# Optimization experiments

Hardware: AMD Instinct MI355X
Metric: run time of the kernel (lower is better)

Reference implementation:

```python
import jax, jax.numpy as jnp
import numpy as np

N, E, G = 100000, 3_200_000, 128   # nodes, edges, graphs in batch
IN, H, C = 16, 64, 4               # in_dim, hidden, num_classes


def setup_inputs() -> dict:
    key = jax.random.key(0)
    ks = jax.random.split(key, 6)
    x = jax.random.normal(ks[0], (N, IN), dtype=jnp.float32)
    edge_index = jax.random.randint(ks[1], (2, E), 0, N, dtype=jnp.int64)
    batch = jnp.sort(jax.random.randint(ks[2], (N,), 0, G, dtype=jnp.int64))
    glorot = lambda k, shp, fan: jax.random.normal(k, shp, jnp.float32) / np.sqrt(fan).astype(np.float32)
    return dict(
        x=x, edge_index=edge_index, batch=batch,
        W1=glorot(ks[3], (IN, H), IN), b1=jnp.zeros((H,), jnp.float32),
        W2=glorot(ks[4], (H, H), H), b2=jnp.zeros((H,), jnp.float32),
        Wl=glorot(ks[5], (H, C), H), bl=jnp.zeros((C,), jnp.float32),
    )


def gcn_conv(x, src, dst, W, b, n):
    """PyG GCNConv: h = D^{-1/2} (A+I) D^{-1/2} (x W) + b, edges incl. self-loops."""
    h = x @ W  # [n, out]
    deg = jax.ops.segment_sum(jnp.ones(src.shape[0], x.dtype), dst, num_segments=n)
    dinv = jnp.where(deg > 0, jax.lax.rsqrt(deg), 0.0)
    norm = dinv[src] * dinv[dst]                       # [E+n]
    out = jax.ops.segment_sum(h[src] * norm[:, None], dst, num_segments=n)
    return out + b


def reference(x, edge_index, batch, W1, b1, W2, b2, Wl, bl):
    n = x.shape[0]
    loops = jnp.arange(n, dtype=edge_index.dtype)      # self-loops (gcn_norm)
    src = jnp.concatenate([edge_index[0], loops])
    dst = jnp.concatenate([edge_index[1], loops])
    h = jax.nn.relu(gcn_conv(x, src, dst, W1, b1, n))
    h = jax.nn.relu(gcn_conv(h, src, dst, W2, b2, n))
    g = jax.ops.segment_sum(h, batch, num_segments=G)  # global_add_pool -> [G, H]
    return g @ Wl + bl                                  # [G, C]
```

## Files before the change

### kernel.cpp

```cpp
#include <hip/hip_runtime.h>
#include <hip/hip_bf16.h>

#define NN 100000
#define EE 3200000
#define GG 128
#define IN_DIM 16
#define HDIM 64
#define CDIM 4

#define RN 256
#define NB ((NN + RN - 1) / RN)
#define CH 8192

typedef unsigned short u16;
typedef unsigned int u32;
typedef __attribute__((ext_vector_type(8))) short bf16x8;
typedef __attribute__((ext_vector_type(4))) float f32x4;

__device__ __forceinline__ float bf_lo(u32 w) { return __uint_as_float(w << 16); }
__device__ __forceinline__ float bf_hi(u32 w) { return __uint_as_float(w & 0xFFFF0000u); }
__device__ __forceinline__ u16 f2bf(float f) {
    u32 x = __float_as_uint(f);
    return (u16)((x + 0x7FFFu + ((x >> 16) & 1u)) >> 16);
}
__device__ __forceinline__ float rdlane(float v, int lane) {
    return __int_as_float(__builtin_amdgcn_readlane(__float_as_int(v), lane));
}


__global__ __launch_bounds__(512) void bhist_k(const int* __restrict__ dst,
                                               int* __restrict__ bcnt) {
    __shared__ int hist[NB];
    int t = threadIdx.x;
    long e0 = (long)blockIdx.x * CH;
    int cnt = (int)min((long)CH, (long)EE - e0);
    for (int i = t; i < NB; i += 512) hist[i] = 0;
    __syncthreads();
    for (int i = t; i < cnt; i += 512) atomicAdd(&hist[dst[e0 + i] >> 8], 1);
    __syncthreads();
    for (int i = t; i < NB; i += 512) {
        int v = hist[i];
        if (v > 0) atomicAdd(&bcnt[i], v);
    }
}

__global__ void bucketscan_k(const int* __restrict__ bcnt, int* __restrict__ bucketBase,
                             int* __restrict__ gcursor) {
    __shared__ int s[512];
    int t = threadIdx.x;
    int c = (t < NB) ? bcnt[t] : 0;
    s[t] = c;
    __syncthreads();
    for (int off = 1; off < 512; off <<= 1) {
        int v = (t >= off) ? s[t - off] : 0;
        __syncthreads();
        s[t] += v;
        __syncthreads();
    }
    if (t < NB) {
        int base = s[t] - c;
        bucketBase[t] = base;
        gcursor[t] = base;
    }
    if (t == 0) bucketBase[NB] = EE;
}


__global__ __launch_bounds__(512) void partition_k(const int* __restrict__ src,
                                                   const int* __restrict__ dst,
                                                   int* __restrict__ gcursor,
                                                   u32* __restrict__ pairs) {
    __shared__ int hist[NB];
    __shared__ int lbase[NB];
    __shared__ int gbase[NB];
    __shared__ int scanbuf[512];
    __shared__ u32 stag[CH];
    __shared__ u16 stagb[CH];
    int t = threadIdx.x;
    long e0 = (long)blockIdx.x * CH;
    int cnt = (int)min((long)CH, (long)EE - e0);

    for (int i = t; i < NB; i += 512) hist[i] = 0;
    __syncthreads();

    int myb[16], myloc[16];
    u32 myp[16];
#pragma unroll
    for (int r = 0; r < 16; ++r) {
        int i = t + (r << 9);
        if (i < cnt) {
            int s = src[e0 + i], d = dst[e0 + i];
            int b = d >> 8;
            myb[r] = b;
            myp[r] = ((u32)s << 8) | (u32)(d & 255);
            myloc[r] = atomicAdd(&hist[b], 1);
        } else {
            myb[r] = -1;
            myloc[r] = 0;
            myp[r] = 0;
        }
    }
    __syncthreads();

    scanbuf[t] = (t < NB) ? hist[t] : 0;
    __syncthreads();
    for (int off = 1; off < 512; off <<= 1) {
        int v = (t >= off) ? scanbuf[t - off] : 0;
        __syncthreads();
        scanbuf[t] += v;
        __syncthreads();
    }
    if (t < NB) {
        lbase[t] = scanbuf[t] - hist[t];
        gbase[t] = (hist[t] > 0) ? atomicAdd(&gcursor[t], hist[t]) : 0;
    }
    __syncthreads();

#pragma unroll
    for (int r = 0; r < 16; ++r) {
        if (myb[r] >= 0) {
            int pos = lbase[myb[r]] + myloc[r];
            stag[pos] = myp[r];
            stagb[pos] = (u16)myb[r];
        }
    }
    __syncthreads();

    for (int i = t; i < cnt; i += 512) {
        int b = stagb[i];
        pairs[gbase[b] + (i - lbase[b])] = stag[i];
    }
}


__global__ __launch_bounds__(512) void csrfill_k(const int* __restrict__ bucketBase,
                                                 const u32* __restrict__ pairs,
                                                 int* __restrict__ rowptr,
                                                 float* __restrict__ dinv,
                                                 int* __restrict__ srcS) {
    __shared__ int sb[256];
    __shared__ int sdeg[256];
    __shared__ int lcur[256];
    int b = blockIdx.x, t = threadIdx.x;
    int n0 = b << 8;
    int gb = bucketBase[b];
    int gend = bucketBase[b + 1];

    if (t < 256) sb[t] = 0;
    __syncthreads();

    for (int idx = gb + t; idx < gend; idx += 512) atomicAdd(&sb[pairs[idx] & 255u], 1);
    __syncthreads();

    int d = (t < 256) ? sb[t] : 0;
    if (t < 256) {
        sdeg[t] = d;
        int n = n0 + t;
        if (n < NN) dinv[n] = rsqrtf((float)(d + 1));
    }
    __syncthreads();
    for (int off = 1; off < 256; off <<= 1) {
        int v = 0;
        if (t < 256 && t >= off) v = sb[t - off];
        __syncthreads();
        if (t < 256) sb[t] += v;
        __syncthreads();
    }
    if (t < 256) {
        int excl = sb[t] - sdeg[t];
        int n = n0 + t;
        if (n < NN) rowptr[n] = gb + excl;
        lcur[t] = excl;
    }
    if (b == 0 && t == 0) rowptr[NN] = EE;
    __syncthreads();

    for (int idx = gb + t; idx < gend; idx += 512) {
        u32 p = pairs[idx];
        int dl = (int)(p & 255u);
        int slot = atomicAdd(&lcur[dl], 1);
        srcS[gb + slot] = (int)(p >> 8);
    }
}


__global__ void xs_k(const float* __restrict__ x, const float* __restrict__ dinv,
                     u16* __restrict__ xs) {
    int i = blockIdx.x * 256 + threadIdx.x;
    if (i >= NN * 4) return;
    int n = i >> 2;
    float dn = dinv[n];
    float4 v = ((const float4*)x)[i];
    u32 p0 = (u32)f2bf(v.x * dn) | ((u32)f2bf(v.y * dn) << 16);
    u32 p1 = (u32)f2bf(v.z * dn) | ((u32)f2bf(v.w * dn) << 16);
    uint2 pk; pk.x = p0; pk.y = p1;
    ((uint2*)xs)[i] = pk;
}

#define ACCUM8(acc, v)                       \
    {                                        \
        acc[0] += bf_lo(v.x);                \
        acc[1] += bf_hi(v.x);                \
        acc[2] += bf_lo(v.y);                \
        acc[3] += bf_hi(v.y);                \
        acc[4] += bf_lo(v.z);                \
        acc[5] += bf_hi(v.z);                \
        acc[6] += bf_lo(v.w);                \
        acc[7] += bf_hi(v.w);                \
    }

#define FOLD3(res, acc, mA, mB, mC)                                   \
    {                                                                 \
        float tj[4], uj[2];                                           \
        _Pragma("unroll")                                             \
        for (int j = 0; j < 4; j++) {                                 \
            float lo = acc[j], hi = acc[j + 4];                       \
            float snd = (lane & mA) ? lo : hi;                        \
            float rcv = __shfl_xor(snd, mA);                          \
            tj[j] = (lane & mA) ? hi + rcv : lo + rcv;                \
        }                                                             \
        _Pragma("unroll")                                             \
        for (int j = 0; j < 2; j++) {                                 \
            float lo = tj[j], hi = tj[j + 2];                         \
            float snd = (lane & mB) ? lo : hi;                        \
            float rcv = __shfl_xor(snd, mB);                          \
            uj[j] = (lane & mB) ? hi + rcv : lo + rcv;                \
        }                                                             \
        {                                                             \
            float lo = uj[0], hi = uj[1];                             \
            float snd = (lane & mC) ? lo : hi;                        \
            float rcv = __shfl_xor(snd, mC);                          \
            res = (lane & mC) ? hi + rcv : lo + rcv;                  \
        }                                                             \
    }


__global__ __launch_bounds__(256) void aggx_k(const u16* __restrict__ xs,
                                              const int* __restrict__ rowptr,
                                              const int* __restrict__ srcS,
                                              const float* __restrict__ dinv,
                                              const float* __restrict__ b1,
                                              const float* __restrict__ W1,
                                              u16* __restrict__ h1d) {
    int t = threadIdx.x;
    int lane = t & 63, w = t >> 6;
    int c = lane & 1, r = lane >> 1;
    int n0 = blockIdx.x * 8 + w * 2;
    int n1 = n0 + 1;

    float w1c[16];
#pragma unroll
    for (int k = 0; k < 16; k++) w1c[k] = W1[k * HDIM + lane];
    float b1l = b1[lane];

    int beg0 = rowptr[n0], end0 = rowptr[n0 + 1], end1 = rowptr[n0 + 2];
    int beg1 = end0;
    float dn0 = dinv[n0], dn1 = dinv[n1];

    float acc0[8] = {0, 0, 0, 0, 0, 0, 0, 0};
    float acc1[8] = {0, 0, 0, 0, 0, 0, 0, 0};
    if (r == 0) {
        uint4 v0 = *(const uint4*)(xs + ((size_t)n0 << 4) + (c << 3));
        uint4 v1 = *(const uint4*)(xs + ((size_t)n1 << 4) + (c << 3));
        ACCUM8(acc0, v0);
        ACCUM8(acc1, v1);
    }
    int itmax = max((end0 - beg0 + 31) >> 5, (end1 - beg1 + 31) >> 5);
    for (int it = 0; it < itmax; ++it) {
        int eA = beg0 + (it << 5) + r;
        int eB = beg1 + (it << 5) + r;
        int iA = srcS[eA < end0 ? eA : beg0];
        int iB = srcS[eB < end1 ? eB : beg1];
        uint4 vA = *(const uint4*)(xs + ((size_t)iA << 4) + (c << 3));
        uint4 vB = *(const uint4*)(xs + ((size_t)iB << 4) + (c << 3));
        if (eA < end0) ACCUM8(acc0, vA);
        if (eB < end1) ACCUM8(acc1, vB);
    }

    float v0, v1;
    FOLD3(v0, acc0, 2, 4, 8);
    FOLD3(v1, acc1, 2, 4, 8);
    v0 += __shfl_xor(v0, 16); v0 += __shfl_xor(v0, 32);
    v1 += __shfl_xor(v1, 16); v1 += __shfl_xor(v1, 32);

    float dot0 = 0.f, dot1 = 0.f;
#pragma unroll
    for (int k = 0; k < 16; k++) {
        int L = ((k >> 3) & 1) | (((k >> 2) & 1) << 1) | (((k >> 1) & 1) << 2) | ((k & 1) << 3);
        dot0 = fmaf(rdlane(v0, L), w1c[k], dot0);
        dot1 = fmaf(rdlane(v1, L), w1c[k], dot1);
    }
    float h0 = fmaxf(fmaf(dot0, dn0, b1l), 0.f);
    float h1 = fmaxf(fmaf(dot1, dn1, b1l), 0.f);

    h1d[(size_t)n0 * HDIM + lane] = f2bf(h0 * dn0);
    h1d[(size_t)n1 * HDIM + lane] = f2bf(h1 * dn1);
}


__global__ __launch_bounds__(256) void gemm_w2_k(const u16* __restrict__ h1d,
                                                 const float* __restrict__ W2,
                                                 u16* __restrict__ h2s) {
    int t = threadIdx.x;
    int lane = t & 63, w = t >> 6;
    int L4 = lane >> 4, L15 = lane & 15;

    bf16x8 bfrag[4][2];
#pragma unroll
    for (int nt = 0; nt < 4; ++nt)
#pragma unroll
        for (int s = 0; s < 2; ++s) {
#pragma unroll
            for (int j = 0; j < 8; ++j) {
                int k = s * 32 + L4 * 8 + j;
                bfrag[nt][s][j] = (short)f2bf(W2[k * HDIM + nt * 16 + L15]);
            }
        }

    int tile0 = (blockIdx.x * 4 + w) * 2;
#pragma unroll
    for (int ti = 0; ti < 2; ++ti) {
        int tile = tile0 + ti;
        if (tile >= NN / 16) break;
        int node = tile * 16 + L15;
        const u16* arow = h1d + (size_t)node * HDIM + L4 * 8;
        bf16x8 a0 = *(const bf16x8*)(arow);
        bf16x8 a1 = *(const bf16x8*)(arow + 32);

        f32x4 c[4];
#pragma unroll
        for (int nt = 0; nt < 4; ++nt) {
            c[nt] = (f32x4){0.f, 0.f, 0.f, 0.f};
            c[nt] = __builtin_amdgcn_mfma_f32_16x16x32_bf16(a0, bfrag[nt][0], c[nt], 0, 0, 0);
            c[nt] = __builtin_amdgcn_mfma_f32_16x16x32_bf16(a1, bfrag[nt][1], c[nt], 0, 0, 0);
        }
#pragma unroll
        for (int q = 0; q < 4; ++q) {
            int row = L4 * 4 + q;
            size_t base = (size_t)(tile * 16 + row) * HDIM + L15;
#pragma unroll
            for (int nt = 0; nt < 4; ++nt) h2s[base + nt * 16] = f2bf(c[nt][q]);
        }
    }
}


__global__ __launch_bounds__(512) void agg_pool_k(const u16* __restrict__ hs,
                                                  const int* __restrict__ rowptr,
                                                  const int* __restrict__ srcS,
                                                  const float* __restrict__ dinv,
                                                  const float* __restrict__ b2,
                                                  const int* __restrict__ batch,
                                                  float* __restrict__ g) {
    __shared__ float gacc[4][HDIM];
    __shared__ int s_g0, s_gmax;
    int t = threadIdx.x;
    int lane = t & 63, w = t >> 6;
    int nbase = blockIdx.x * 32;

    if (t < 4 * HDIM) gacc[t >> 6][t & 63] = 0.f;
    if (t == 0) { s_g0 = batch[nbase]; s_gmax = 0; }
    __syncthreads();
    int g0 = s_g0;

    int r = lane >> 3, c = lane & 7;
    int f = (c << 3) + ((lane & 8) ? 4 : 0) + ((lane & 16) ? 2 : 0) + ((lane & 32) ? 1 : 0);
    float b2f = b2[f];

    for (int ni = 0; ni < 4; ++ni) {
        int n = nbase + w * 4 + ni;
        int beg = rowptr[n], end = rowptr[n + 1];
        float acc[8] = {0.f, 0.f, 0.f, 0.f, 0.f, 0.f, 0.f, 0.f};
        if (r == 0) {
            uint4 v = *(const uint4*)(hs + ((size_t)n << 6) + (c << 3));
            ACCUM8(acc, v);
        }
        for (int e0 = beg; e0 < end; e0 += 32) {
            int eA = e0 + r, eB = eA + 8, eC = eA + 16, eD = eA + 24;
            int iA = srcS[eA < end ? eA : beg];
            int iB = srcS[eB < end ? eB : beg];
            int iC = srcS[eC < end ? eC : beg];
            int iD = srcS[eD < end ? eD : beg];
            uint4 vA = *(const uint4*)(hs + ((size_t)iA << 6) + (c << 3));
            uint4 vB = *(const uint4*)(hs + ((size_t)iB << 6) + (c << 3));
            uint4 vC = *(const uint4*)(hs + ((size_t)iC << 6) + (c << 3));
            uint4 vD = *(const uint4*)(hs + ((size_t)iD << 6) + (c << 3));
            if (eA < end) ACCUM8(acc, vA);
            if (eB < end) ACCUM8(acc, vB);
            if (eC < end) ACCUM8(acc, vC);
            if (eD < end) ACCUM8(acc, vD);
        }
        float red;
        FOLD3(red, acc, 8, 16, 32);
        float v = fmaf(red, dinv[n], b2f);
        v = fmaxf(v, 0.f);
        int gi = batch[n] - g0;
        if (gi < 4) {
            atomicAdd(&gacc[gi][f], v);
            if (lane == 0) atomicMax(&s_gmax, gi);
        } else {
            unsafeAtomicAdd(&g[(size_t)batch[n] * HDIM + f], v);
        }
    }
    __syncthreads();
    if (t < 4 * HDIM) {
        int slot = t >> 6, ff = t & 63;
        if (slot <= s_gmax) unsafeAtomicAdd(&g[(size_t)(g0 + slot) * HDIM + ff], gacc[slot][ff]);
    }
}

__global__ void final_k(const float* __restrict__ g, const float* __restrict__ Wl,
                        const float* __restrict__ bl, float* __restrict__ out) {
    int t = threadIdx.x;
    int gi = t >> 2, cc = t & 3;
    float acc = bl[cc];
#pragma unroll
    for (int k = 0; k < HDIM; k++) acc = fmaf(g[gi * HDIM + k], Wl[k * CDIM + cc], acc);
    out[gi * CDIM + cc] = acc;
}


extern "C" void kernel_launch(void* const* d_in, const int* in_sizes, int n_in,
                              void* d_out, int out_size, void* d_ws, size_t ws_size,
                              hipStream_t stream) {
    const float* x   = (const float*)d_in[0];
    const int*   ei  = (const int*)d_in[1];
    const int*   src = ei;
    const int*   dst = ei + EE;
    const int*   batch = (const int*)d_in[2];
    const float* W1 = (const float*)d_in[3];
    const float* b1 = (const float*)d_in[4];
    const float* W2 = (const float*)d_in[5];
    const float* b2 = (const float*)d_in[6];
    const float* Wl = (const float*)d_in[7];
    const float* bl = (const float*)d_in[8];
    float* out = (float*)d_out;

    char* w = (char*)d_ws;
    auto alloc = [&](size_t bytes) -> char* {
        char* p = w;
        w += (bytes + 255) & ~(size_t)255;
        return p;
    };
    int*   bcnt       = (int*)alloc((size_t)NB * 4);
    int*   bucketBase = (int*)alloc((size_t)(NB + 1) * 4);
    int*   gcursor    = (int*)alloc((size_t)NB * 4);
    u32*   pairs      = (u32*)alloc((size_t)EE * 4);
    int*   srcS       = (int*)alloc((size_t)EE * 4);
    int*   rowptr     = (int*)alloc((size_t)(NN + 1) * 4);
    float* dinv       = (float*)alloc((size_t)NN * 4);
    u16*   xs         = (u16*)alloc((size_t)NN * IN_DIM * 2);
    u16*   h1d        = (u16*)alloc((size_t)NN * HDIM * 2);
    u16*   h2s        = (u16*)alloc((size_t)NN * HDIM * 2);
    float* g          = (float*)alloc((size_t)GG * HDIM * 4);

    hipMemsetAsync(bcnt, 0, (size_t)NB * 4, stream);
    hipMemsetAsync(g, 0, (size_t)GG * HDIM * 4, stream);

    const int NCHUNK = (EE + CH - 1) / CH;
    bhist_k<<<NCHUNK, 512, 0, stream>>>(dst, bcnt);
    bucketscan_k<<<1, 512, 0, stream>>>(bcnt, bucketBase, gcursor);
    partition_k<<<NCHUNK, 512, 0, stream>>>(src, dst, gcursor, pairs);
    csrfill_k<<<NB, 512, 0, stream>>>(bucketBase, pairs, rowptr, dinv, srcS);

    xs_k<<<(NN * 4 + 255) / 256, 256, 0, stream>>>(x, dinv, xs);
    aggx_k<<<NN / 8, 256, 0, stream>>>(xs, rowptr, srcS, dinv, b1, W1, h1d);
    gemm_w2_k<<<(NN / 16 + 7) / 8, 256, 0, stream>>>(h1d, W2, h2s);
    agg_pool_k<<<(NN + 31) / 32, 512, 0, stream>>>(h2s, rowptr, srcS, dinv, b2, batch, g);
    final_k<<<1, 512, 0, stream>>>(g, Wl, bl, out);
}
```

Baseline: 179.2 us.

## Sort CSR edges by source slice and aggregate slice-by-slice for cache locality

The CSR build now counts edges per destination in eight source-index slices (p>>22) and orders each row by slice, storing packed per-node slice counts. The second aggregation walks all four nodes of a warp slice by slice, so concurrent gathers hit a narrower source range of h2s and reuse L2 better. In exchange it adds shared-memory atomics on a larger histogram, an extra 8-byte-per-node array, and finer 8-edge gather loops with less memory-level parallelism per iteration. It also assumes per-slice counts fit in 8 bits and that NSL=7 covers every source slice.

```diff
diff --git a/kernel.cpp b/kernel.cpp
--- a/kernel.cpp
+++ b/kernel.cpp
@@ -11,9 +11,11 @@
 #define RN 256
 #define NB ((NN + RN - 1) / RN)
 #define CH 8192
+#define NSL 7
 
 typedef unsigned short u16;
 typedef unsigned int u32;
+typedef unsigned long long u64;
 typedef __attribute__((ext_vector_type(8))) short bf16x8;
 typedef __attribute__((ext_vector_type(4))) float f32x4;
 
@@ -137,26 +139,43 @@
                                                  const u32* __restrict__ pairs,
                                                  int* __restrict__ rowptr,
                                                  float* __restrict__ dinv,
-                                                 int* __restrict__ srcS) {
+                                                 int* __restrict__ srcS,
+                                                 u64* __restrict__ sliceCnt) {
+    __shared__ int cnt2[256 * 8];
+    __shared__ int cur2[256 * 8];
     __shared__ int sb[256];
     __shared__ int sdeg[256];
-    __shared__ int lcur[256];
     int b = blockIdx.x, t = threadIdx.x;
     int n0 = b << 8;
     int gb = bucketBase[b];
     int gend = bucketBase[b + 1];
 
-    if (t < 256) sb[t] = 0;
-    __syncthreads();
-
-    for (int idx = gb + t; idx < gend; idx += 512) atomicAdd(&sb[pairs[idx] & 255u], 1);
-    __syncthreads();
-
-    int d = (t < 256) ? sb[t] : 0;
+    for (int i = t; i < 2048; i += 512) cnt2[i] = 0;
+    __syncthreads();
+
+    for (int idx = gb + t; idx < gend; idx += 512) {
+        u32 p = pairs[idx];
+        atomicAdd(&cnt2[((p & 255u) << 3) + (p >> 22)], 1);
+    }
+    __syncthreads();
+
     if (t < 256) {
-        sdeg[t] = d;
+        int run = 0;
+        u64 pk = 0;
+#pragma unroll
+        for (int s = 0; s < 8; s++) {
+            int cs = cnt2[(t << 3) + s];
+            cur2[(t << 3) + s] = run;
+            run += cs;
+            pk |= ((u64)(u32)cs) << (8 * s);
+        }
+        sb[t] = run;
+        sdeg[t] = run;
         int n = n0 + t;
-        if (n < NN) dinv[n] = rsqrtf((float)(d + 1));
+        if (n < NN) {
+            dinv[n] = rsqrtf((float)(run + 1));
+            sliceCnt[n] = pk;
+        }
     }
     __syncthreads();
     for (int off = 1; off < 256; off <<= 1) {
@@ -170,15 +189,15 @@
         int excl = sb[t] - sdeg[t];
         int n = n0 + t;
         if (n < NN) rowptr[n] = gb + excl;
-        lcur[t] = excl;
+#pragma unroll
+        for (int s = 0; s < 8; s++) cur2[(t << 3) + s] += excl;
     }
     if (b == 0 && t == 0) rowptr[NN] = EE;
     __syncthreads();
 
     for (int idx = gb + t; idx < gend; idx += 512) {
         u32 p = pairs[idx];
-        int dl = (int)(p & 255u);
-        int slot = atomicAdd(&lcur[dl], 1);
+        int slot = atomicAdd(&cur2[((p & 255u) << 3) + (p >> 22)], 1);
         srcS[gb + slot] = (int)(p >> 8);
     }
 }
@@ -351,6 +370,7 @@
                                                   const float* __restrict__ dinv,
                                                   const float* __restrict__ b2,
                                                   const int* __restrict__ batch,
+                                                  const u64* __restrict__ sliceCnt,
                                                   float* __restrict__ g) {
     __shared__ float gacc[4][HDIM];
     __shared__ int s_g0, s_gmax;
@@ -367,31 +387,43 @@
     int f = (c << 3) + ((lane & 8) ? 4 : 0) + ((lane & 16) ? 2 : 0) + ((lane & 32) ? 1 : 0);
     float b2f = b2[f];
 
+    int nw = nbase + w * 4;
+    float acc[4][8];
+    u64 cnts[4];
+    int cur[4];
+#pragma unroll
     for (int ni = 0; ni < 4; ++ni) {
-        int n = nbase + w * 4 + ni;
-        int beg = rowptr[n], end = rowptr[n + 1];
-        float acc[8] = {0.f, 0.f, 0.f, 0.f, 0.f, 0.f, 0.f, 0.f};
+#pragma unroll
+        for (int j = 0; j < 8; j++) acc[ni][j] = 0.f;
+        int n = nw + ni;
+        cur[ni] = rowptr[n];
+        cnts[ni] = sliceCnt[n];
         if (r == 0) {
             uint4 v = *(const uint4*)(hs + ((size_t)n << 6) + (c << 3));
-            ACCUM8(acc, v);
-        }
-        for (int e0 = beg; e0 < end; e0 += 32) {
-            int eA = e0 + r, eB = eA + 8, eC = eA + 16, eD = eA + 24;
-            int iA = srcS[eA < end ? eA : beg];
-            int iB = srcS[eB < end ? eB : beg];
-            int iC = srcS[eC < end ? eC : beg];
-            int iD = srcS[eD < end ? eD : beg];
-            uint4 vA = *(const uint4*)(hs + ((size_t)iA << 6) + (c << 3));
-            uint4 vB = *(const uint4*)(hs + ((size_t)iB << 6) + (c << 3));
-            uint4 vC = *(const uint4*)(hs + ((size_t)iC << 6) + (c << 3));
-            uint4 vD = *(const uint4*)(hs + ((size_t)iD << 6) + (c << 3));
-            if (eA < end) ACCUM8(acc, vA);
-            if (eB < end) ACCUM8(acc, vB);
-            if (eC < end) ACCUM8(acc, vC);
-            if (eD < end) ACCUM8(acc, vD);
-        }
+            ACCUM8(acc[ni], v);
+        }
+    }
+
+    for (int s = 0; s < NSL; ++s) {
+#pragma unroll
+        for (int ni = 0; ni < 4; ++ni) {
+            int cnt = (int)((cnts[ni] >> (8 * s)) & 255ull);
+            int e0 = cur[ni], e1 = e0 + cnt;
+            for (int e = e0; e < e1; e += 8) {
+                int eA = e + r;
+                int iA = srcS[eA < e1 ? eA : e0];
+                uint4 v = *(const uint4*)(hs + ((size_t)iA << 6) + (c << 3));
+                if (eA < e1) ACCUM8(acc[ni], v);
+            }
+            cur[ni] = e1;
+        }
+    }
+
+#pragma unroll
+    for (int ni = 0; ni < 4; ++ni) {
         float red;
-        FOLD3(red, acc, 8, 16, 32);
+        FOLD3(red, acc[ni], 8, 16, 32);
+        int n = nw + ni;
         float v = fmaf(red, dinv[n], b2f);
         v = fmaxf(v, 0.f);
         int gi = batch[n] - g0;
@@ -449,6 +481,7 @@
     int*   srcS       = (int*)alloc((size_t)EE * 4);
     int*   rowptr     = (int*)alloc((size_t)(NN + 1) * 4);
     float* dinv       = (float*)alloc((size_t)NN * 4);
+    u64*   sliceCnt   = (u64*)alloc((size_t)NN * 8);
     u16*   xs         = (u16*)alloc((size_t)NN * IN_DIM * 2);
     u16*   h1d        = (u16*)alloc((size_t)NN * HDIM * 2);
     u16*   h2s        = (u16*)alloc((size_t)NN * HDIM * 2);
@@ -461,11 +494,11 @@
     bhist_k<<<NCHUNK, 512, 0, stream>>>(dst, bcnt);
     bucketscan_k<<<1, 512, 0, stream>>>(bcnt, bucketBase, gcursor);
     partition_k<<<NCHUNK, 512, 0, stream>>>(src, dst, gcursor, pairs);
-    csrfill_k<<<NB, 512, 0, stream>>>(bucketBase, pairs, rowptr, dinv, srcS);
+    csrfill_k<<<NB, 512, 0, stream>>>(bucketBase, pairs, rowptr, dinv, srcS, sliceCnt);
 
     xs_k<<<(NN * 4 + 255) / 256, 256, 0, stream>>>(x, dinv, xs);
     aggx_k<<<NN / 8, 256, 0, stream>>>(xs, rowptr, srcS, dinv, b1, W1, h1d);
     gemm_w2_k<<<(NN / 16 + 7) / 8, 256, 0, stream>>>(h1d, W2, h2s);
-    agg_pool_k<<<(NN + 31) / 32, 512, 0, stream>>>(h2s, rowptr, srcS, dinv, b2, batch, g);
+    agg_pool_k<<<(NN + 31) / 32, 512, 0, stream>>>(h2s, rowptr, srcS, dinv, b2, batch, sliceCnt, g);
     final_k<<<1, 512, 0, stream>>>(g, Wl, bl, out);
 }
```

Result: slower. 307.0 us (+71.3%).

## Fuse x scaling into CSR fill and W2 GEMM into layer-1 aggregation

Applied to the files above, without the earlier changes.

The separate xs_k kernel is folded into csrfill_k, which now converts x to bf16 scaled by the per-node inverse degree it has just computed and kept in shared memory. The layer-1 aggregation kernel now handles 16 nodes per 512-thread block, stages the 16x64 hidden tile in LDS and has one wave run the MFMA with W2 directly. This drops the h1d intermediate round trip through global memory and two kernel launches. In exchange, every block converts W2 into bf16 fragments, and 7 of the 8 waves sit idle during the MFMA step.

```diff
diff --git a/kernel.cpp b/kernel.cpp
--- a/kernel.cpp
+++ b/kernel.cpp
@@ -135,16 +135,20 @@
 
 __global__ __launch_bounds__(512) void csrfill_k(const int* __restrict__ bucketBase,
                                                  const u32* __restrict__ pairs,
+                                                 const float* __restrict__ x,
                                                  int* __restrict__ rowptr,
                                                  float* __restrict__ dinv,
-                                                 int* __restrict__ srcS) {
+                                                 int* __restrict__ srcS,
+                                                 u16* __restrict__ xs) {
     __shared__ int sb[256];
     __shared__ int sdeg[256];
     __shared__ int lcur[256];
+    __shared__ float sdinv[256];
     int b = blockIdx.x, t = threadIdx.x;
     int n0 = b << 8;
     int gb = bucketBase[b];
     int gend = bucketBase[b + 1];
+    int nvalid = min(256, NN - n0);
 
     if (t < 256) sb[t] = 0;
     __syncthreads();
@@ -155,8 +159,10 @@
     int d = (t < 256) ? sb[t] : 0;
     if (t < 256) {
         sdeg[t] = d;
+        float dn = rsqrtf((float)(d + 1));
+        sdinv[t] = dn;
         int n = n0 + t;
-        if (n < NN) dinv[n] = rsqrtf((float)(d + 1));
+        if (n < NN) dinv[n] = dn;
     }
     __syncthreads();
     for (int off = 1; off < 256; off <<= 1) {
@@ -181,20 +187,16 @@
         int slot = atomicAdd(&lcur[dl], 1);
         srcS[gb + slot] = (int)(p >> 8);
     }
-}
-
-
-__global__ void xs_k(const float* __restrict__ x, const float* __restrict__ dinv,
-                     u16* __restrict__ xs) {
-    int i = blockIdx.x * 256 + threadIdx.x;
-    if (i >= NN * 4) return;
-    int n = i >> 2;
-    float dn = dinv[n];
-    float4 v = ((const float4*)x)[i];
-    u32 p0 = (u32)f2bf(v.x * dn) | ((u32)f2bf(v.y * dn) << 16);
-    u32 p1 = (u32)f2bf(v.z * dn) | ((u32)f2bf(v.w * dn) << 16);
-    uint2 pk; pk.x = p0; pk.y = p1;
-    ((uint2*)xs)[i] = pk;
+
+    for (int q = t; q < nvalid * 4; q += 512) {
+        int nloc = q >> 2;
+        float dn = sdinv[nloc];
+        float4 v = ((const float4*)x)[(size_t)n0 * 4 + q];
+        u32 p0 = (u32)f2bf(v.x * dn) | ((u32)f2bf(v.y * dn) << 16);
+        u32 p1 = (u32)f2bf(v.z * dn) | ((u32)f2bf(v.w * dn) << 16);
+        uint2 pk; pk.x = p0; pk.y = p1;
+        ((uint2*)xs)[(size_t)n0 * 4 + q] = pk;
+    }
 }
 
 #define ACCUM8(acc, v)                       \
@@ -235,18 +237,35 @@
     }
 
 
-__global__ __launch_bounds__(256) void aggx_k(const u16* __restrict__ xs,
-                                              const int* __restrict__ rowptr,
-                                              const int* __restrict__ srcS,
-                                              const float* __restrict__ dinv,
-                                              const float* __restrict__ b1,
-                                              const float* __restrict__ W1,
-                                              u16* __restrict__ h1d) {
+__global__ __launch_bounds__(512) void aggxg_k(const u16* __restrict__ xs,
+                                               const int* __restrict__ rowptr,
+                                               const int* __restrict__ srcS,
+                                               const float* __restrict__ dinv,
+                                               const float* __restrict__ b1,
+                                               const float* __restrict__ W1,
+                                               const float* __restrict__ W2,
+                                               u16* __restrict__ h2s) {
+    __shared__ u16 atile[16][72];
     int t = threadIdx.x;
     int lane = t & 63, w = t >> 6;
     int c = lane & 1, r = lane >> 1;
-    int n0 = blockIdx.x * 8 + w * 2;
+    int nb = blockIdx.x * 16;
+    int n0 = nb + w * 2;
     int n1 = n0 + 1;
+    int L4 = lane >> 4, L15 = lane & 15;
+
+    bf16x8 bfrag[4][2];
+    if (w == 0) {
+#pragma unroll
+        for (int nt = 0; nt < 4; ++nt)
+#pragma unroll
+            for (int s = 0; s < 2; ++s)
+#pragma unroll
+                for (int j = 0; j < 8; ++j) {
+                    int k = s * 32 + L4 * 8 + j;
+                    bfrag[nt][s][j] = (short)f2bf(W2[k * HDIM + nt * 16 + L15]);
+                }
+    }
 
     float w1c[16];
 #pragma unroll
@@ -293,53 +312,26 @@
     float h0 = fmaxf(fmaf(dot0, dn0, b1l), 0.f);
     float h1 = fmaxf(fmaf(dot1, dn1, b1l), 0.f);
 
-    h1d[(size_t)n0 * HDIM + lane] = f2bf(h0 * dn0);
-    h1d[(size_t)n1 * HDIM + lane] = f2bf(h1 * dn1);
-}
-
-
-__global__ __launch_bounds__(256) void gemm_w2_k(const u16* __restrict__ h1d,
-                                                 const float* __restrict__ W2,
-                                                 u16* __restrict__ h2s) {
-    int t = threadIdx.x;
-    int lane = t & 63, w = t >> 6;
-    int L4 = lane >> 4, L15 = lane & 15;
-
-    bf16x8 bfrag[4][2];
-#pragma unroll
-    for (int nt = 0; nt < 4; ++nt)
-#pragma unroll
-        for (int s = 0; s < 2; ++s) {
-#pragma unroll
-            for (int j = 0; j < 8; ++j) {
-                int k = s * 32 + L4 * 8 + j;
-                bfrag[nt][s][j] = (short)f2bf(W2[k * HDIM + nt * 16 + L15]);
-            }
-        }
-
-    int tile0 = (blockIdx.x * 4 + w) * 2;
-#pragma unroll
-    for (int ti = 0; ti < 2; ++ti) {
-        int tile = tile0 + ti;
-        if (tile >= NN / 16) break;
-        int node = tile * 16 + L15;
-        const u16* arow = h1d + (size_t)node * HDIM + L4 * 8;
-        bf16x8 a0 = *(const bf16x8*)(arow);
-        bf16x8 a1 = *(const bf16x8*)(arow + 32);
-
-        f32x4 c[4];
+    atile[w * 2][lane] = f2bf(h0 * dn0);
+    atile[w * 2 + 1][lane] = f2bf(h1 * dn1);
+    __syncthreads();
+
+    if (w == 0) {
+        bf16x8 a0 = *(const bf16x8*)&atile[L15][L4 * 8];
+        bf16x8 a1 = *(const bf16x8*)&atile[L15][L4 * 8 + 32];
+        f32x4 cc[4];
 #pragma unroll
         for (int nt = 0; nt < 4; ++nt) {
-            c[nt] = (f32x4){0.f, 0.f, 0.f, 0.f};
-            c[nt] = __builtin_amdgcn_mfma_f32_16x16x32_bf16(a0, bfrag[nt][0], c[nt], 0, 0, 0);
-            c[nt] = __builtin_amdgcn_mfma_f32_16x16x32_bf16(a1, bfrag[nt][1], c[nt], 0, 0, 0);
+            cc[nt] = (f32x4){0.f, 0.f, 0.f, 0.f};
+            cc[nt] = __builtin_amdgcn_mfma_f32_16x16x32_bf16(a0, bfrag[nt][0], cc[nt], 0, 0, 0);
+            cc[nt] = __builtin_amdgcn_mfma_f32_16x16x32_bf16(a1, bfrag[nt][1], cc[nt], 0, 0, 0);
         }
 #pragma unroll
         for (int q = 0; q < 4; ++q) {
             int row = L4 * 4 + q;
-            size_t base = (size_t)(tile * 16 + row) * HDIM + L15;
-#pragma unroll
-            for (int nt = 0; nt < 4; ++nt) h2s[base + nt * 16] = f2bf(c[nt][q]);
+            size_t base = (size_t)(nb + row) * HDIM + L15;
+#pragma unroll
+            for (int nt = 0; nt < 4; ++nt) h2s[base + nt * 16] = f2bf(cc[nt][q]);
         }
     }
 }
@@ -450,7 +442,6 @@
     int*   rowptr     = (int*)alloc((size_t)(NN + 1) * 4);
     float* dinv       = (float*)alloc((size_t)NN * 4);
     u16*   xs         = (u16*)alloc((size_t)NN * IN_DIM * 2);
-    u16*   h1d        = (u16*)alloc((size_t)NN * HDIM * 2);
     u16*   h2s        = (u16*)alloc((size_t)NN * HDIM * 2);
     float* g          = (float*)alloc((size_t)GG * HDIM * 4);
 
@@ -461,11 +452,9 @@
     bhist_k<<<NCHUNK, 512, 0, stream>>>(dst, bcnt);
     bucketscan_k<<<1, 512, 0, stream>>>(bcnt, bucketBase, gcursor);
     partition_k<<<NCHUNK, 512, 0, stream>>>(src, dst, gcursor, pairs);
-    csrfill_k<<<NB, 512, 0, stream>>>(bucketBase, pairs, rowptr, dinv, srcS);
-
-    xs_k<<<(NN * 4 + 255) / 256, 256, 0, stream>>>(x, dinv, xs);
-    aggx_k<<<NN / 8, 256, 0, stream>>>(xs, rowptr, srcS, dinv, b1, W1, h1d);
-    gemm_w2_k<<<(NN / 16 + 7) / 8, 256, 0, stream>>>(h1d, W2, h2s);
+    csrfill_k<<<NB, 512, 0, stream>>>(bucketBase, pairs, x, rowptr, dinv, srcS, xs);
+
+    aggxg_k<<<NN / 16, 512, 0, stream>>>(xs, rowptr, srcS, dinv, b1, W1, W2, h2s);
     agg_pool_k<<<(NN + 31) / 32, 512, 0, stream>>>(h2s, rowptr, srcS, dinv, b2, batch, g);
     final_k<<<1, 512, 0, stream>>>(g, Wl, bl, out);
 }
```

After: 195.5 us. 1.09x slower.

## Fuse CSR build and feature scaling into one cooperative kernel with grid syncs

Applied to the files above, without the earlier changes.

Replaces the bucket-histogram, bucket-scan, partition, CSR-fill and feature-scaling kernels with one cooperatively launched kernel. The stages are separated by grid-wide syncs. Each block reads its edge chunk once and uses the resulting local histogram both for the global bucket counts and for the partition, which drops the separate read of the dst array. Each block also converts its own node range of x using degree-normalisation values kept in shared memory, and four kernel launch gaps go away. In exchange the whole grid must be co-resident, and it pays several grid barriers with a single block doing the bucket scan while the rest wait.

```diff
diff --git a/kernel.cpp b/kernel.cpp
--- a/kernel.cpp
+++ b/kernel.cpp
@@ -1,5 +1,8 @@
 #include <hip/hip_runtime.h>
 #include <hip/hip_bf16.h>
+#include <hip/hip_cooperative_groups.h>
+
+namespace cg = cooperative_groups;
 
 #define NN 100000
 #define EE 3200000
@@ -28,61 +31,36 @@
 }
 
 
-__global__ __launch_bounds__(512) void bhist_k(const int* __restrict__ dst,
-                                               int* __restrict__ bcnt) {
-    __shared__ int hist[NB];
-    int t = threadIdx.x;
-    long e0 = (long)blockIdx.x * CH;
-    int cnt = (int)min((long)CH, (long)EE - e0);
-    for (int i = t; i < NB; i += 512) hist[i] = 0;
-    __syncthreads();
-    for (int i = t; i < cnt; i += 512) atomicAdd(&hist[dst[e0 + i] >> 8], 1);
-    __syncthreads();
-    for (int i = t; i < NB; i += 512) {
-        int v = hist[i];
-        if (v > 0) atomicAdd(&bcnt[i], v);
-    }
-}
-
-__global__ void bucketscan_k(const int* __restrict__ bcnt, int* __restrict__ bucketBase,
-                             int* __restrict__ gcursor) {
-    __shared__ int s[512];
-    int t = threadIdx.x;
-    int c = (t < NB) ? bcnt[t] : 0;
-    s[t] = c;
-    __syncthreads();
-    for (int off = 1; off < 512; off <<= 1) {
-        int v = (t >= off) ? s[t - off] : 0;
-        __syncthreads();
-        s[t] += v;
-        __syncthreads();
-    }
-    if (t < NB) {
-        int base = s[t] - c;
-        bucketBase[t] = base;
-        gcursor[t] = base;
-    }
-    if (t == 0) bucketBase[NB] = EE;
-}
-
-
-__global__ __launch_bounds__(512) void partition_k(const int* __restrict__ src,
-                                                   const int* __restrict__ dst,
-                                                   int* __restrict__ gcursor,
-                                                   u32* __restrict__ pairs) {
+__global__ __launch_bounds__(512) void build_k(const int* __restrict__ src,
+                                               const int* __restrict__ dst,
+                                               const float* __restrict__ x,
+                                               int* __restrict__ bcnt,
+                                               int* __restrict__ bucketBase,
+                                               int* __restrict__ gcursor,
+                                               u32* __restrict__ pairs,
+                                               int* __restrict__ rowptr,
+                                               float* __restrict__ dinv,
+                                               int* __restrict__ srcS,
+                                               u16* __restrict__ xs) {
     __shared__ int hist[NB];
     __shared__ int lbase[NB];
     __shared__ int gbase[NB];
     __shared__ int scanbuf[512];
     __shared__ u32 stag[CH];
     __shared__ u16 stagb[CH];
+    __shared__ int sb[256];
+    __shared__ int sdeg[256];
+    __shared__ int lcur[256];
+    __shared__ float sdinv[256];
+
+    cg::grid_group grid = cg::this_grid();
     int t = threadIdx.x;
-    long e0 = (long)blockIdx.x * CH;
+    int b = blockIdx.x;
+    long e0 = (long)b * CH;
     int cnt = (int)min((long)CH, (long)EE - e0);
 
     for (int i = t; i < NB; i += 512) hist[i] = 0;
     __syncthreads();
-
     int myb[16], myloc[16];
     u32 myp[16];
 #pragma unroll
@@ -90,10 +68,10 @@
         int i = t + (r << 9);
         if (i < cnt) {
             int s = src[e0 + i], d = dst[e0 + i];
-            int b = d >> 8;
-            myb[r] = b;
+            int bb = d >> 8;
+            myb[r] = bb;
             myp[r] = ((u32)s << 8) | (u32)(d & 255);
-            myloc[r] = atomicAdd(&hist[b], 1);
+            myloc[r] = atomicAdd(&hist[bb], 1);
         } else {
             myb[r] = -1;
             myloc[r] = 0;
@@ -101,6 +79,32 @@
         }
     }
     __syncthreads();
+    for (int i = t; i < NB; i += 512) {
+        int v = hist[i];
+        if (v > 0) atomicAdd(&bcnt[i], v);
+    }
+    __threadfence();
+    grid.sync();
+
+    if (b == 0) {
+        int c2 = (t < NB) ? bcnt[t] : 0;
+        scanbuf[t] = c2;
+        __syncthreads();
+        for (int off = 1; off < 512; off <<= 1) {
+            int v = (t >= off) ? scanbuf[t - off] : 0;
+            __syncthreads();
+            scanbuf[t] += v;
+            __syncthreads();
+        }
+        if (t < NB) {
+            int base = scanbuf[t] - c2;
+            bucketBase[t] = base;
+            gcursor[t] = base;
+        }
+        if (t == 0) bucketBase[NB] = EE;
+    }
+    __threadfence();
+    grid.sync();
 
     scanbuf[t] = (t < NB) ? hist[t] : 0;
     __syncthreads();
@@ -115,7 +119,6 @@
         gbase[t] = (hist[t] > 0) ? atomicAdd(&gcursor[t], hist[t]) : 0;
     }
     __syncthreads();
-
 #pragma unroll
     for (int r = 0; r < 16; ++r) {
         if (myb[r] >= 0) {
@@ -125,38 +128,29 @@
         }
     }
     __syncthreads();
-
     for (int i = t; i < cnt; i += 512) {
-        int b = stagb[i];
-        pairs[gbase[b] + (i - lbase[b])] = stag[i];
-    }
-}
-
-
-__global__ __launch_bounds__(512) void csrfill_k(const int* __restrict__ bucketBase,
-                                                 const u32* __restrict__ pairs,
-                                                 int* __restrict__ rowptr,
-                                                 float* __restrict__ dinv,
-                                                 int* __restrict__ srcS) {
-    __shared__ int sb[256];
-    __shared__ int sdeg[256];
-    __shared__ int lcur[256];
-    int b = blockIdx.x, t = threadIdx.x;
+        int bb = stagb[i];
+        pairs[gbase[bb] + (i - lbase[bb])] = stag[i];
+    }
+    __threadfence();
+    grid.sync();
+
     int n0 = b << 8;
     int gb = bucketBase[b];
     int gend = bucketBase[b + 1];
+    int nvalid = min(256, NN - n0);
 
     if (t < 256) sb[t] = 0;
     __syncthreads();
-
     for (int idx = gb + t; idx < gend; idx += 512) atomicAdd(&sb[pairs[idx] & 255u], 1);
     __syncthreads();
-
     int d = (t < 256) ? sb[t] : 0;
     if (t < 256) {
         sdeg[t] = d;
+        float dn = rsqrtf((float)(d + 1));
+        sdinv[t] = dn;
         int n = n0 + t;
-        if (n < NN) dinv[n] = rsqrtf((float)(d + 1));
+        if (n < NN) dinv[n] = dn;
     }
     __syncthreads();
     for (int off = 1; off < 256; off <<= 1) {
@@ -174,27 +168,21 @@
     }
     if (b == 0 && t == 0) rowptr[NN] = EE;
     __syncthreads();
-
     for (int idx = gb + t; idx < gend; idx += 512) {
         u32 p = pairs[idx];
         int dl = (int)(p & 255u);
         int slot = atomicAdd(&lcur[dl], 1);
         srcS[gb + slot] = (int)(p >> 8);
     }
-}
-
-
-__global__ void xs_k(const float* __restrict__ x, const float* __restrict__ dinv,
-                     u16* __restrict__ xs) {
-    int i = blockIdx.x * 256 + threadIdx.x;
-    if (i >= NN * 4) return;
-    int n = i >> 2;
-    float dn = dinv[n];
-    float4 v = ((const float4*)x)[i];
-    u32 p0 = (u32)f2bf(v.x * dn) | ((u32)f2bf(v.y * dn) << 16);
-    u32 p1 = (u32)f2bf(v.z * dn) | ((u32)f2bf(v.w * dn) << 16);
-    uint2 pk; pk.x = p0; pk.y = p1;
-    ((uint2*)xs)[i] = pk;
+    for (int q = t; q < nvalid * 4; q += 512) {
+        int nloc = q >> 2;
+        float dn = sdinv[nloc];
+        float4 v = ((const float4*)x)[(size_t)n0 * 4 + q];
+        u32 p0 = (u32)f2bf(v.x * dn) | ((u32)f2bf(v.y * dn) << 16);
+        u32 p1 = (u32)f2bf(v.z * dn) | ((u32)f2bf(v.w * dn) << 16);
+        uint2 pk; pk.x = p0; pk.y = p1;
+        ((uint2*)xs)[(size_t)n0 * 4 + q] = pk;
+    }
 }
 
 #define ACCUM8(acc, v)                       \
@@ -457,15 +445,15 @@
     hipMemsetAsync(bcnt, 0, (size_t)NB * 4, stream);
     hipMemsetAsync(g, 0, (size_t)GG * HDIM * 4, stream);
 
-    const int NCHUNK = (EE + CH - 1) / CH;
-    bhist_k<<<NCHUNK, 512, 0, stream>>>(dst, bcnt);
-    bucketscan_k<<<1, 512, 0, stream>>>(bcnt, bucketBase, gcursor);
-    partition_k<<<NCHUNK, 512, 0, stream>>>(src, dst, gcursor, pairs);
-    csrfill_k<<<NB, 512, 0, stream>>>(bucketBase, pairs, rowptr, dinv, srcS);
-
-    xs_k<<<(NN * 4 + 255) / 256, 256, 0, stream>>>(x, dinv, xs);
+    {
+        void* args[] = {(void*)&src, (void*)&dst, (void*)&x, (void*)&bcnt,
+                        (void*)&bucketBase, (void*)&gcursor, (void*)&pairs,
+                        (void*)&rowptr, (void*)&dinv, (void*)&srcS, (void*)&xs};
+        hipLaunchCooperativeKernel((void*)build_k, dim3(NB), dim3(512), args, 0, stream);
+    }
+
     aggx_k<<<NN / 8, 256, 0, stream>>>(xs, rowptr, srcS, dinv, b1, W1, h1d);
     gemm_w2_k<<<(NN / 16 + 7) / 8, 256, 0, stream>>>(h1d, W2, h2s);
-    agg_pool_k<<<(NN + 31) / 32, 512, 0, stream>>>(h2s, rowptr, srcS, dinv, b2, batch, g);
+    agg_pool_k<<<NN / 32, 512, 0, stream>>>(h2s, rowptr, srcS, dinv, b2, batch, g);
     final_k<<<1, 512, 0, stream>>>(g, Wl, bl, out);
 }
```

New measurement: 486.1 us. 2.71x slower.
